# Performance work log

Hardware: AMD Instinct MI355X
Metric: run time of the kernel (lower is better)

The kernel has to match this reference:

```python
import jax, jax.numpy as jnp
import numpy as np

BATCH = 65536
DIM = 512
NUM_CLASSES = 1000
NUM_OLD = 500  # old_classes == set(range(NUM_OLD))


def setup_inputs() -> dict:
    key = jax.random.key(0)
    k1, k2, k3 = jax.random.split(key, 3)
    embeddings = jax.random.normal(k1, (BATCH, DIM), dtype=jnp.float32)
    centroids = jax.random.normal(k2, (NUM_CLASSES, DIM), dtype=jnp.float32)
    labels = jax.random.randint(k3, (BATCH,), 0, NUM_CLASSES, dtype=jnp.int64 if jax.config.jax_enable_x64 else jnp.int32)
    return {"embeddings": embeddings, "centroids": centroids, "labels": labels, "num_old": NUM_OLD}


def reference(embeddings, centroids, labels, num_old):
    # Fused gather + per-sample MSE + masked mean (replaces the per-sample Python loop).
    gathered = centroids[labels]                                  # [B, D]
    per_sample = jnp.mean((embeddings - gathered) ** 2, axis=-1)  # [B], F.mse_loss per sample
    # Original accumulates dis.detach(): the loss value carries no gradient.
    per_sample = jax.lax.stop_gradient(per_sample)
    mask = labels < num_old                                       # label in old_classes
    count = jnp.sum(mask)
    total = jnp.sum(jnp.where(mask, per_sample, jnp.float32(0.0)))
    # if count == 0: return raw (zero) loss, else mean
    loss = jnp.where(count == 0, total, total / jnp.maximum(count, 1).astype(total.dtype))
    return loss
```

## Files before the change

kernel.cpp:

```cpp
#include <hip/hip_runtime.h>

constexpr int kDim = 512;
constexpr int kF4PerRow = kDim / 4;

__global__ void zero_ws_kernel(float* g_sum, unsigned int* g_cnt) {
    *g_sum = 0.0f;
    *g_cnt = 0u;
}

__global__ __launch_bounds__(256) void mse_masked_kernel(
    const float* __restrict__ emb,
    const float* __restrict__ cen,
    const int* __restrict__ labels,
    const int* __restrict__ num_old_p,
    int batch,
    float* __restrict__ g_sum,
    unsigned int* __restrict__ g_cnt)
{
    const int num_old = *num_old_p;
    const int lane = threadIdx.x & 63;
    const int wid  = threadIdx.x >> 6;
    const int gwave = blockIdx.x * (blockDim.x >> 6) + wid;
    const int nwave = gridDim.x * (blockDim.x >> 6);

    const float4* __restrict__ emb4 = (const float4*)emb;
    const float4* __restrict__ cen4 = (const float4*)cen;

    float acc = 0.0f;
    unsigned int cnt = 0;

    for (int s = gwave; s < batch; s += nwave) {
        const int lab = labels[s];
        if (lab >= num_old) continue;
        cnt++;

        const float4* er = emb4 + (size_t)s   * kF4PerRow;
        const float4* cr = cen4 + (size_t)lab * kF4PerRow;
        float4 e0 = er[lane];
        float4 e1 = er[lane + 64];
        float4 c0 = cr[lane];
        float4 c1 = cr[lane + 64];

        float d, t;
        d = e0.x - c0.x; t  = d * d;
        d = e0.y - c0.y; t += d * d;
        d = e0.z - c0.z; t += d * d;
        d = e0.w - c0.w; t += d * d;
        d = e1.x - c1.x; t += d * d;
        d = e1.y - c1.y; t += d * d;
        d = e1.z - c1.z; t += d * d;
        d = e1.w - c1.w; t += d * d;
        acc += t;
    }

    #pragma unroll
    for (int off = 32; off > 0; off >>= 1)
        acc += __shfl_xor(acc, off, 64);

    __shared__ float        s_sum[4];
    __shared__ unsigned int s_cnt[4];
    if (lane == 0) { s_sum[wid] = acc; s_cnt[wid] = cnt; }
    __syncthreads();

    if (threadIdx.x == 0) {
        float        bs = 0.0f;
        unsigned int bc = 0u;
        const int nw = blockDim.x >> 6;
        for (int i = 0; i < nw; ++i) { bs += s_sum[i]; bc += s_cnt[i]; }
        atomicAdd(g_sum, bs);
        atomicAdd(g_cnt, bc);
    }
}

__global__ void finalize_kernel(const float* __restrict__ g_sum,
                                const unsigned int* __restrict__ g_cnt,
                                float* __restrict__ out)
{
    const float total = (*g_sum) * (1.0f / (float)kDim);
    const unsigned int c = *g_cnt;
    out[0] = (c == 0u) ? total : total / (float)c;
}

extern "C" void kernel_launch(void* const* d_in, const int* in_sizes, int n_in,
                              void* d_out, int out_size, void* d_ws, size_t ws_size,
                              hipStream_t stream) {
    const float* emb       = (const float*)d_in[0];
    const float* cen       = (const float*)d_in[1];
    const int*   labels    = (const int*)d_in[2];
    const int*   num_old_p = (const int*)d_in[3];

    const int batch = in_sizes[2];

    float*        g_sum = (float*)d_ws;
    unsigned int* g_cnt = (unsigned int*)((char*)d_ws + sizeof(float));

    zero_ws_kernel<<<1, 1, 0, stream>>>(g_sum, g_cnt);

    const int blocks = 1024;
    mse_masked_kernel<<<blocks, 256, 0, stream>>>(emb, cen, labels, num_old_p,
                                                  batch, g_sum, g_cnt);

    finalize_kernel<<<1, 1, 0, stream>>>(g_sum, g_cnt, (float*)d_out);
}
```

Before: 206.9 us.

## Batch label loads via ballot, issue four row gathers at once, drop atomics

Each wave now loads 64 labels at once and uses a ballot mask to walk the selected samples. It issues loads for four rows and their centroids together to raise memory-level parallelism, instead of doing one dependent label load per row. Global atomics and the zeroing kernel are replaced by per-block partial sums that a 256-thread finalize kernel reduces, which removes one launch. The grid shrinks to 256 blocks, so fewer waves may be resident, and register pressure rises from the 16 in-flight float4 loads.

Result: faster. 186.1 us (median of 2 runs) (-10.0%).

```diff
diff --git a/kernel.cpp b/kernel.cpp
--- a/kernel.cpp
+++ b/kernel.cpp
@@ -3,9 +3,17 @@
 constexpr int kDim = 512;
 constexpr int kF4PerRow = kDim / 4;
 
-__global__ void zero_ws_kernel(float* g_sum, unsigned int* g_cnt) {
-    *g_sum = 0.0f;
-    *g_cnt = 0u;
+__device__ __forceinline__ float sqdiff8(float4 e0, float4 e1, float4 c0, float4 c1) {
+    float d, t;
+    d = e0.x - c0.x; t  = d * d;
+    d = e0.y - c0.y; t += d * d;
+    d = e0.z - c0.z; t += d * d;
+    d = e0.w - c0.w; t += d * d;
+    d = e1.x - c1.x; t += d * d;
+    d = e1.y - c1.y; t += d * d;
+    d = e1.z - c1.z; t += d * d;
+    d = e1.w - c1.w; t += d * d;
+    return t;
 }
 
 __global__ __launch_bounds__(256) void mse_masked_kernel(
@@ -14,14 +22,15 @@
     const int* __restrict__ labels,
     const int* __restrict__ num_old_p,
     int batch,
-    float* __restrict__ g_sum,
-    unsigned int* __restrict__ g_cnt)
+    float* __restrict__ ws_sum,
+    unsigned int* __restrict__ ws_cnt)
 {
     const int num_old = *num_old_p;
     const int lane = threadIdx.x & 63;
     const int wid  = threadIdx.x >> 6;
-    const int gwave = blockIdx.x * (blockDim.x >> 6) + wid;
-    const int nwave = gridDim.x * (blockDim.x >> 6);
+    const int wpb  = blockDim.x >> 6;
+    const int gwave = blockIdx.x * wpb + wid;
+    const int nwave = gridDim.x * wpb;
 
     const float4* __restrict__ emb4 = (const float4*)emb;
     const float4* __restrict__ cen4 = (const float4*)cen;
@@ -29,28 +38,54 @@
     float acc = 0.0f;
     unsigned int cnt = 0;
 
-    for (int s = gwave; s < batch; s += nwave) {
-        const int lab = labels[s];
-        if (lab >= num_old) continue;
-        cnt++;
+    for (int chunk = gwave * 64; chunk < batch; chunk += nwave * 64) {
+        const int idx = chunk + lane;
+        const int mylab = (idx < batch) ? labels[idx] : 0x7fffffff;
+        unsigned long long m = __ballot(mylab < num_old);
+        cnt += (unsigned int)__popcll(m);
 
-        const float4* er = emb4 + (size_t)s   * kF4PerRow;
-        const float4* cr = cen4 + (size_t)lab * kF4PerRow;
-        float4 e0 = er[lane];
-        float4 e1 = er[lane + 64];
-        float4 c0 = cr[lane];
-        float4 c1 = cr[lane + 64];
+        while (__popcll(m) >= 4) {
+            const int b0 = __builtin_ctzll(m); m &= m - 1;
+            const int b1 = __builtin_ctzll(m); m &= m - 1;
+            const int b2 = __builtin_ctzll(m); m &= m - 1;
+            const int b3 = __builtin_ctzll(m); m &= m - 1;
+            const int l0 = __shfl(mylab, b0, 64);
+            const int l1 = __shfl(mylab, b1, 64);
+            const int l2 = __shfl(mylab, b2, 64);
+            const int l3 = __shfl(mylab, b3, 64);
 
-        float d, t;
-        d = e0.x - c0.x; t  = d * d;
-        d = e0.y - c0.y; t += d * d;
-        d = e0.z - c0.z; t += d * d;
-        d = e0.w - c0.w; t += d * d;
-        d = e1.x - c1.x; t += d * d;
-        d = e1.y - c1.y; t += d * d;
-        d = e1.z - c1.z; t += d * d;
-        d = e1.w - c1.w; t += d * d;
-        acc += t;
+            const float4* e0p = emb4 + (size_t)(chunk + b0) * kF4PerRow;
+            const float4* e1p = emb4 + (size_t)(chunk + b1) * kF4PerRow;
+            const float4* e2p = emb4 + (size_t)(chunk + b2) * kF4PerRow;
+            const float4* e3p = emb4 + (size_t)(chunk + b3) * kF4PerRow;
+            const float4* c0p = cen4 + (size_t)l0 * kF4PerRow;
+            const float4* c1p = cen4 + (size_t)l1 * kF4PerRow;
+            const float4* c2p = cen4 + (size_t)l2 * kF4PerRow;
+            const float4* c3p = cen4 + (size_t)l3 * kF4PerRow;
+
+            float4 ea0 = e0p[lane], eb0 = e0p[lane + 64];
+            float4 ea1 = e1p[lane], eb1 = e1p[lane + 64];
+            float4 ea2 = e2p[lane], eb2 = e2p[lane + 64];
+            float4 ea3 = e3p[lane], eb3 = e3p[lane + 64];
+            float4 ca0 = c0p[lane], cb0 = c0p[lane + 64];
+            float4 ca1 = c1p[lane], cb1 = c1p[lane + 64];
+            float4 ca2 = c2p[lane], cb2 = c2p[lane + 64];
+            float4 ca3 = c3p[lane], cb3 = c3p[lane + 64];
+
+            acc += sqdiff8(ea0, eb0, ca0, cb0);
+            acc += sqdiff8(ea1, eb1, ca1, cb1);
+            acc += sqdiff8(ea2, eb2, ca2, cb2);
+            acc += sqdiff8(ea3, eb3, ca3, cb3);
+        }
+        while (m) {
+            const int b = __builtin_ctzll(m); m &= m - 1;
+            const int l = __shfl(mylab, b, 64);
+            const float4* ep = emb4 + (size_t)(chunk + b) * kF4PerRow;
+            const float4* cp = cen4 + (size_t)l * kF4PerRow;
+            float4 e0 = ep[lane], e1 = ep[lane + 64];
+            float4 c0 = cp[lane], c1 = cp[lane + 64];
+            acc += sqdiff8(e0, e1, c0, c1);
+        }
     }
 
     #pragma unroll
@@ -65,20 +100,38 @@
     if (threadIdx.x == 0) {
         float        bs = 0.0f;
         unsigned int bc = 0u;
-        const int nw = blockDim.x >> 6;
-        for (int i = 0; i < nw; ++i) { bs += s_sum[i]; bc += s_cnt[i]; }
-        atomicAdd(g_sum, bs);
-        atomicAdd(g_cnt, bc);
+        for (int i = 0; i < wpb; ++i) { bs += s_sum[i]; bc += s_cnt[i]; }
+        ws_sum[blockIdx.x] = bs;
+        ws_cnt[blockIdx.x] = bc;
     }
 }
 
-__global__ void finalize_kernel(const float* __restrict__ g_sum,
-                                const unsigned int* __restrict__ g_cnt,
-                                float* __restrict__ out)
+__global__ __launch_bounds__(256) void finalize_kernel(
+    const float* __restrict__ ws_sum,
+    const unsigned int* __restrict__ ws_cnt,
+    int nparts,
+    float* __restrict__ out)
 {
-    const float total = (*g_sum) * (1.0f / (float)kDim);
-    const unsigned int c = *g_cnt;
-    out[0] = (c == 0u) ? total : total / (float)c;
+    const int t = threadIdx.x;
+    float        s = (t < nparts) ? ws_sum[t] : 0.0f;
+    unsigned int c = (t < nparts) ? ws_cnt[t] : 0u;
+
+    #pragma unroll
+    for (int off = 32; off > 0; off >>= 1) {
+        s += __shfl_xor(s, off, 64);
+        c += __shfl_xor(c, off, 64);
+    }
+    __shared__ float        ls[4];
+    __shared__ unsigned int lc[4];
+    const int lane = t & 63, wid = t >> 6;
+    if (lane == 0) { ls[wid] = s; lc[wid] = c; }
+    __syncthreads();
+    if (t == 0) {
+        float        ts = ls[0] + ls[1] + ls[2] + ls[3];
+        unsigned int tc = lc[0] + lc[1] + lc[2] + lc[3];
+        const float total = ts * (1.0f / (float)kDim);
+        out[0] = (tc == 0u) ? total : total / (float)tc;
+    }
 }
 
 extern "C" void kernel_launch(void* const* d_in, const int* in_sizes, int n_in,
@@ -91,14 +144,11 @@
 
     const int batch = in_sizes[2];
 
-    float*        g_sum = (float*)d_ws;
-    unsigned int* g_cnt = (unsigned int*)((char*)d_ws + sizeof(float));
+    const int blocks = 256;
+    float*        ws_sum = (float*)d_ws;
+    unsigned int* ws_cnt = (unsigned int*)((char*)d_ws + blocks * sizeof(float));
 
-    zero_ws_kernel<<<1, 1, 0, stream>>>(g_sum, g_cnt);
-
-    const int blocks = 1024;
     mse_masked_kernel<<<blocks, 256, 0, stream>>>(emb, cen, labels, num_old_p,
-                                                  batch, g_sum, g_cnt);
-
-    finalize_kernel<<<1, 1, 0, stream>>>(g_sum, g_cnt, (float*)d_out);
+                                                  batch, ws_sum, ws_cnt);
+    finalize_kernel<<<1, 256, 0, stream>>>(ws_sum, ws_cnt, blocks, (float*)d_out);
 }
```
